# Kernel optimization log

Measured on AMD Instinct MI355X. Metric: run time of the kernel, lower is better.

## Reference

```python
import jax, jax.numpy as jnp
import numpy as np
from jax import lax

DIM = 512
HEADS = 8


def _branch(x, w1, wd):
    # 1x1 pointwise conv (no bias)
    y = jnp.einsum('oc,bchw->bohw', w1, x)
    # ReflectionPad2d(2)
    y = jnp.pad(y, ((0, 0), (0, 0), (2, 2), (2, 2)), mode='reflect')
    # depthwise 3x3, dilation 2, valid padding (net: same spatial size)
    y = lax.conv_general_dilated(
        y, wd, window_strides=(1, 1), padding='VALID', rhs_dilation=(2, 2),
        dimension_numbers=('NCHW', 'OIHW', 'NCHW'), feature_group_count=y.shape[1])
    return y


def setup_inputs() -> dict:
    key = jax.random.key(0)
    ks = jax.random.split(key, 8)
    s = 0.02
    style_feat = jax.random.normal(ks[0], (16, DIM, 64, 64), dtype=jnp.float32)
    fw1 = jax.random.normal(ks[1], (DIM, DIM), dtype=jnp.float32) * s
    fwd_ = jax.random.normal(ks[2], (DIM, 1, 3, 3), dtype=jnp.float32) * s
    gw1 = jax.random.normal(ks[3], (DIM, DIM), dtype=jnp.float32) * s
    gwd = jax.random.normal(ks[4], (DIM, 1, 3, 3), dtype=jnp.float32) * s
    hw1 = jax.random.normal(ks[5], (DIM, DIM), dtype=jnp.float32) * s
    hwd = jax.random.normal(ks[6], (DIM, 1, 3, 3), dtype=jnp.float32) * s
    ow = jax.random.normal(ks[7], (DIM, DIM), dtype=jnp.float32) * s
    temperature = jnp.ones((HEADS, 1, 1), dtype=jnp.float32)
    return dict(style_feat=style_feat, fw1=fw1, fwd_=fwd_, gw1=gw1, gwd=gwd,
                hw1=hw1, hwd=hwd, ow=ow, temperature=temperature)


def reference(style_feat, fw1, fwd_, gw1, gwd, hw1, hwd, ow, temperature):
    B, C, H, W = style_feat.shape
    cph = C // HEADS
    f_x = _branch(style_feat, fw1, fwd_)
    g_x = _branch(style_feat, gw1, gwd)
    h_x = _branch(style_feat, hw1, hwd)
    q = f_x.reshape(B, HEADS, cph, H * W)
    k = g_x.reshape(B, HEADS, cph, H * W)
    v = h_x.reshape(B, HEADS, cph, H * W)
    # channel-wise attention: [B,h,cph,cph]
    energy = jnp.einsum('bhcn,bhdn->bhcd', q, k)
    attn = jax.nn.softmax(energy * temperature[None], axis=-1)
    out = jnp.einsum('bhcd,bhdn->bhcn', attn, v).reshape(B, C, H, W)
    out = jnp.einsum('oc,bchw->bohw', ow, out)
    return out + style_feat
```

## Files before the change

kernel.cpp:

```cpp
#include <hip/hip_runtime.h>

typedef unsigned short u16;
typedef __bf16 bf8_t __attribute__((ext_vector_type(8)));
typedef short short8 __attribute__((ext_vector_type(8)));
typedef float f32x4 __attribute__((ext_vector_type(4)));

#define DEV __device__ __forceinline__

DEV u16 f2bf(float x) {
  unsigned u = __builtin_bit_cast(unsigned, x);
  return (u16)((u + 0x7FFFu + ((u >> 16) & 1u)) >> 16);
}
DEV float bf2f(u16 x) {
  unsigned u = (unsigned)x << 16;
  return __builtin_bit_cast(float, u);
}

DEV void gload16(const u16* g, u16* l) {
  __builtin_amdgcn_global_load_lds((__attribute__((address_space(1))) void*)(g),
                                   (__attribute__((address_space(3))) void*)(l), 16, 0, 0);
}

__global__ void k_wconv(const float* __restrict__ f, const float* __restrict__ g,
                        const float* __restrict__ h, u16* __restrict__ out) {
  int i = blockIdx.x * 256 + threadIdx.x;
  float v;
  if (i < 262144) v = f[i];
  else if (i < 524288) v = g[i - 262144];
  else v = h[i - 524288];
  out[i] = f2bf(v);
}

__global__ __launch_bounds__(256) void k_xt(const float* __restrict__ style, u16* __restrict__ Xt) {
  __shared__ float t[32][33];
  int b = blockIdx.z, c0 = blockIdx.y * 32, n0 = blockIdx.x * 32;
  int tid = threadIdx.x, lr = tid >> 5, lc = tid & 31;
  const float* src = style + ((size_t)b * 512 + c0) * 4096 + n0;
#pragma unroll
  for (int it = 0; it < 4; ++it) {
    int r = it * 8 + lr;
    t[r][lc] = src[(size_t)r * 4096 + lc];
  }
  __syncthreads();
  u16* dst = Xt + ((size_t)b * 4096 + n0) * 512 + c0;
#pragma unroll
  for (int it = 0; it < 4; ++it) {
    int n = it * 8 + lr;
    dst[(size_t)n * 512 + lc] = f2bf(t[lc][n]);
  }
}

DEV void stage_tile(const u16* __restrict__ src, int row0, int kb,
                    u16* lds, int wave, int lane) {
#pragma unroll
  for (int qq = 0; qq < 2; ++qq) {
    int idx = (wave * 2 + qq) * 64 + lane;
    int r = idx >> 2;
    int cb = (idx & 3) * 8;
    gload16(src + (size_t)(row0 + r) * 512 + (kb + cb),
            lds + (wave * 2 + qq) * 512);
  }
}

__global__ __launch_bounds__(256, 2) void k_gemm_branch(
    const u16* __restrict__ Wall, const u16* __restrict__ Xt, u16* __restrict__ Y) {
  int bid = blockIdx.x;
  int xcd = bid & 7, idx = bid >> 3;
  int bh = idx / 384;
  int r = idx - bh * 384;
  int b = xcd * 2 + bh;
  int nt = r / 12, mt = r - nt * 12;
  int M0 = mt * 128, N0 = nt * 128;
  const u16* A = Wall;
  const u16* B = Xt + (size_t)b * (4096 * 512);
  u16* C = Y + (size_t)b * (1536 * 4096);
  int tid = threadIdx.x, wave = tid >> 6, lane = tid & 63;
  int wm = wave >> 1, wn = wave & 1;
  __shared__ __align__(16) u16 lA[2][128 * 32];
  __shared__ __align__(16) u16 lB[2][128 * 32];
  f32x4 acc[4][4];
#pragma unroll
  for (int m = 0; m < 4; ++m)
#pragma unroll
    for (int n = 0; n < 4; ++n) acc[m][n] = (f32x4){0.f, 0.f, 0.f, 0.f};
  stage_tile(A, M0, 0, &lA[0][0], wave, lane);
  stage_tile(B, N0, 0, &lB[0][0], wave, lane);
  __syncthreads();
  int lrow = lane & 15, lk = (lane >> 4) * 8;
#pragma unroll 2
  for (int kt = 0; kt < 16; ++kt) {
    int cur = kt & 1;
    if (kt < 15) {
      stage_tile(A, M0, (kt + 1) * 32, &lA[cur ^ 1][0], wave, lane);
      stage_tile(B, N0, (kt + 1) * 32, &lB[cur ^ 1][0], wave, lane);
    }
    bf8_t af[4], bff[4];
#pragma unroll
    for (int m = 0; m < 4; ++m)
      af[m] = *(const bf8_t*)&lA[cur][(wm * 64 + m * 16 + lrow) * 32 + lk];
#pragma unroll
    for (int n = 0; n < 4; ++n)
      bff[n] = *(const bf8_t*)&lB[cur][(wn * 64 + n * 16 + lrow) * 32 + lk];
#pragma unroll
    for (int m = 0; m < 4; ++m)
#pragma unroll
      for (int n = 0; n < 4; ++n)
        acc[m][n] = __builtin_amdgcn_mfma_f32_16x16x32_bf16(af[m], bff[n], acc[m][n], 0, 0, 0);
    __syncthreads();
  }
  int orow = (lane >> 4) * 4, ocol = lane & 15;
#pragma unroll
  for (int m = 0; m < 4; ++m)
#pragma unroll
    for (int n = 0; n < 4; ++n) {
      int row = M0 + wm * 64 + m * 16 + orow;
      int col = N0 + wn * 64 + n * 16 + ocol;
      u16* cp = C + (size_t)row * 4096 + col;
#pragma unroll
      for (int i = 0; i < 4; ++i) cp[(size_t)i * 4096] = f2bf(acc[m][n][i]);
    }
}

template <typename F>
DEV void dw_row(const u16* plane, const float* w9, int y, F&& store) {
  short8 raw[3][8];
#pragma unroll
  for (int i = 0; i < 3; ++i) {
    int yy = y + 2 * i - 2;
    yy = yy < 0 ? -yy : (yy > 63 ? 126 - yy : yy);
    const short8* rp = (const short8*)(plane + yy * 64);
#pragma unroll
    for (int ch = 0; ch < 8; ++ch) raw[i][ch] = rp[ch];
  }
#pragma unroll
  for (int g = 0; g < 4; ++g) {
    float fr[3][20];
#pragma unroll
    for (int t = 0; t < 20; ++t) {
      int p = g * 16 - 2 + t;
      int rp2 = p < 0 ? -p : (p > 63 ? 126 - p : p);
#pragma unroll
      for (int i = 0; i < 3; ++i)
        fr[i][t] = bf2f((u16)raw[i][rp2 >> 3][rp2 & 7]);
    }
    float o[16];
#pragma unroll
    for (int e = 0; e < 16; ++e) {
      float s = 0.f;
#pragma unroll
      for (int i = 0; i < 3; ++i)
#pragma unroll
        for (int j = 0; j < 3; ++j)
          s += w9[i * 3 + j] * fr[i][e + 2 * j];
      o[e] = s;
    }
    store(g, o);
  }
}

__global__ __launch_bounds__(256, 2) void k_dwE(const u16* __restrict__ Y,
    const float* __restrict__ fwd, const float* __restrict__ gwd, float* __restrict__ E) {
  int band = blockIdx.x, h = blockIdx.y, b = blockIdx.z;
  __shared__ __align__(16) u16 qbuf[64 * 256];
  __shared__ __align__(16) u16 kbuf[64 * 256];
  int tid = threadIdx.x;
  int c = ((tid >> 5) << 3) | (tid & 7);
  int yl = (tid >> 3) & 3;
  int wv = tid >> 6, lane = tid & 63;
  int lrow = lane & 15, lkg = lane >> 4;
  const u16* qp = Y + ((size_t)b * 1536 + h * 64 + c) * 4096;
  const u16* kp = Y + ((size_t)b * 1536 + 512 + h * 64 + c) * 4096;
  float wq9[9], wk9[9];
#pragma unroll
  for (int t = 0; t < 9; ++t) {
    wq9[t] = fwd[(h * 64 + c) * 9 + t];
    wk9[t] = gwd[(h * 64 + c) * 9 + t];
  }
  f32x4 acc[4];
#pragma unroll
  for (int n = 0; n < 4; ++n) acc[n] = (f32x4){0.f, 0.f, 0.f, 0.f};
  char* qrow = (char*)qbuf + c * 512;
  char* krow = (char*)kbuf + c * 512;
  int c7 = c & 7;
#pragma unroll 1
  for (int sb = 0; sb < 4; ++sb) {
    int y = band * 16 + sb * 4 + yl;
    dw_row(qp, wq9, y, [&](int g, const float* o) {
      short8 s0, s1;
#pragma unroll
      for (int e = 0; e < 8; ++e) { s0[e] = (short)f2bf(o[e]); s1[e] = (short)f2bf(o[e + 8]); }
      int ch0 = yl * 8 + g * 2;
      *(short8*)(qrow + 16 * (ch0 ^ c7)) = s0;
      *(short8*)(qrow + 16 * ((ch0 + 1) ^ c7)) = s1;
    });
    dw_row(kp, wk9, y, [&](int g, const float* o) {
      short8 s0, s1;
#pragma unroll
      for (int e = 0; e < 8; ++e) { s0[e] = (short)f2bf(o[e]); s1[e] = (short)f2bf(o[e + 8]); }
      int ch0 = yl * 8 + g * 2;
      *(short8*)(krow + 16 * (ch0 ^ c7)) = s0;
      *(short8*)(krow + 16 * ((ch0 + 1) ^ c7)) = s1;
    });
    __syncthreads();
    const char* qb = (const char*)qbuf + (wv * 16 + lrow) * 512;
    int ca7 = (wv * 16 + lrow) & 7;
#pragma unroll
    for (int ks = 0; ks < 8; ++ks) {
      bf8_t aF = *(const bf8_t*)(qb + 16 * ((ks * 4 + lkg) ^ ca7));
#pragma unroll
      for (int n = 0; n < 4; ++n) {
        int cb = n * 16 + lrow;
        bf8_t bF = *(const bf8_t*)((const char*)kbuf + cb * 512 + 16 * ((ks * 4 + lkg) ^ (cb & 7)));
        acc[n] = __builtin_amdgcn_mfma_f32_16x16x32_bf16(aF, bF, acc[n], 0, 0, 0);
      }
    }
    __syncthreads();
  }
  float* Eo = E + (((size_t)band * 16 + b) * 8 + h) * 4096;
  int orow = (lane >> 4) * 4, ocol = lane & 15;
#pragma unroll
  for (int n = 0; n < 4; ++n)
#pragma unroll
    for (int i = 0; i < 4; ++i)
      Eo[(wv * 16 + orow + i) * 64 + n * 16 + ocol] = acc[n][i];
}

__global__ __launch_bounds__(256, 2) void k_dwV(const u16* __restrict__ Y,
    const float* __restrict__ hwd, u16* __restrict__ Vt) {
  int band = blockIdx.x, ct = blockIdx.y, b = blockIdx.z;
  __shared__ float vb[256 * 68];
  int tid = threadIdx.x;
  int c = ((tid >> 5) << 3) | (tid & 7);
  int yl = (tid >> 3) & 3;
  int cg = tid & 7;
  int cglob = ct * 64 + c;
  const u16* plane = Y + ((size_t)b * 1536 + 1024 + cglob) * 4096;
  float w9[9];
#pragma unroll
  for (int t = 0; t < 9; ++t) w9[t] = hwd[cglob * 9 + t];
#pragma unroll 1
  for (int sb = 0; sb < 4; ++sb) {
    int y = band * 16 + sb * 4 + yl;
    dw_row(plane, w9, y, [&](int g, const float* o) {
#pragma unroll
      for (int e = 0; e < 16; ++e)
        vb[((g * 16 + e) * 4 + yl) * 68 + c] = o[e];
    });
    __syncthreads();
#pragma unroll
    for (int k = 0; k < 8; ++k) {
      int np = (tid >> 3) + 32 * k;
      int x = np >> 2, yy = np & 3;
      int ng = (band * 16 + sb * 4 + yy) * 64 + x;
      f32x4 r0 = *(const f32x4*)&vb[np * 68 + cg * 8];
      f32x4 r1 = *(const f32x4*)&vb[np * 68 + cg * 8 + 4];
      short8 s;
#pragma unroll
      for (int e = 0; e < 4; ++e) { s[e] = (short)f2bf(r0[e]); s[e + 4] = (short)f2bf(r1[e]); }
      *(short8*)(Vt + ((size_t)b * 4096 + ng) * 512 + ct * 64 + cg * 8) = s;
    }
    __syncthreads();
  }
}

__global__ __launch_bounds__(64) void k_softmax(float* __restrict__ E, const float* __restrict__ temp) {
  int bh = blockIdx.x;
  int b = bh >> 3, h = bh & 7;
  int c = threadIdx.x;
  float* p0 = E + (((size_t)b * 8 + h) * 64 + c) * 64;
  float tv = temp[h];
  float e[64];
  float mx = -1e30f;
#pragma unroll
  for (int d = 0; d < 64; ++d) {
    float v = (p0[d] + p0[d + 524288] + p0[d + 1048576] + p0[d + 1572864]) * tv;
    e[d] = v;
    mx = fmaxf(mx, v);
  }
  float s = 0.f;
#pragma unroll
  for (int d = 0; d < 64; ++d) { float v = __expf(e[d] - mx); e[d] = v; s += v; }
  float inv = 1.f / s;
#pragma unroll
  for (int d = 0; d < 64; ++d) p0[d] = e[d] * inv;
}

__global__ __launch_bounds__(256) void k_m2(const float* __restrict__ E, const float* __restrict__ ow,
                                            u16* __restrict__ M2) {
  int og = blockIdx.x, h = blockIdx.y, b = blockIdx.z;
  __shared__ float at[4096];
  int tid = threadIdx.x;
  const float* attn = E + ((size_t)b * 8 + h) * 4096;
  for (int v = tid; v < 4096; v += 256) at[v] = attn[v];
  __syncthreads();
  int o = og * 64 + (tid >> 2), dq = (tid & 3) * 16;
  const float* owr = ow + (size_t)o * 512 + h * 64;
  float acc[16];
#pragma unroll
  for (int e = 0; e < 16; ++e) acc[e] = 0.f;
  for (int cc = 0; cc < 64; ++cc) {
    float wv = owr[cc];
#pragma unroll
    for (int e = 0; e < 16; ++e) acc[e] += wv * at[cc * 64 + dq + e];
  }
  u16* dst = M2 + ((size_t)b * 512 + o) * 512 + h * 64 + dq;
  short8 s0, s1;
#pragma unroll
  for (int e = 0; e < 8; ++e) { s0[e] = (short)f2bf(acc[e]); s1[e] = (short)f2bf(acc[e + 8]); }
  *(short8*)dst = s0;
  *(short8*)(dst + 8) = s1;
}

__global__ __launch_bounds__(256, 2) void k_gemm_final(
    const u16* __restrict__ M2, const u16* __restrict__ Vt,
    const float* __restrict__ style, float* __restrict__ out) {
  int b = blockIdx.z;
  const u16* A = M2 + (size_t)b * (512 * 512);
  const u16* B = Vt + (size_t)b * (4096 * 512);
  const float* st = style + (size_t)b * (512 * 4096);
  float* op = out + (size_t)b * (512 * 4096);
  int M0 = blockIdx.y * 128, N0 = blockIdx.x * 128;
  int tid = threadIdx.x, wave = tid >> 6, lane = tid & 63;
  int wm = wave >> 1, wn = wave & 1;
  __shared__ __align__(16) u16 lA[2][128 * 32];
  __shared__ __align__(16) u16 lB[2][128 * 32];
  f32x4 acc[4][4];
#pragma unroll
  for (int m = 0; m < 4; ++m)
#pragma unroll
    for (int n = 0; n < 4; ++n) acc[m][n] = (f32x4){0.f, 0.f, 0.f, 0.f};
  stage_tile(A, M0, 0, &lA[0][0], wave, lane);
  stage_tile(B, N0, 0, &lB[0][0], wave, lane);
  __syncthreads();
  int lrow = lane & 15, lk = (lane >> 4) * 8;
#pragma unroll 2
  for (int kt = 0; kt < 16; ++kt) {
    int cur = kt & 1;
    if (kt < 15) {
      stage_tile(A, M0, (kt + 1) * 32, &lA[cur ^ 1][0], wave, lane);
      stage_tile(B, N0, (kt + 1) * 32, &lB[cur ^ 1][0], wave, lane);
    }
    bf8_t af[4], bff[4];
#pragma unroll
    for (int m = 0; m < 4; ++m)
      af[m] = *(const bf8_t*)&lA[cur][(wm * 64 + m * 16 + lrow) * 32 + lk];
#pragma unroll
    for (int n = 0; n < 4; ++n)
      bff[n] = *(const bf8_t*)&lB[cur][(wn * 64 + n * 16 + lrow) * 32 + lk];
#pragma unroll
    for (int m = 0; m < 4; ++m)
#pragma unroll
      for (int n = 0; n < 4; ++n)
        acc[m][n] = __builtin_amdgcn_mfma_f32_16x16x32_bf16(af[m], bff[n], acc[m][n], 0, 0, 0);
    __syncthreads();
  }
  int orow = (lane >> 4) * 4, ocol = lane & 15;
#pragma unroll
  for (int m = 0; m < 4; ++m)
#pragma unroll
    for (int n = 0; n < 4; ++n) {
      int row = M0 + wm * 64 + m * 16 + orow;
      int col = N0 + wn * 64 + n * 16 + ocol;
      float* cp = op + (size_t)row * 4096 + col;
      const float* sp = st + (size_t)row * 4096 + col;
#pragma unroll
      for (int i = 0; i < 4; ++i) cp[(size_t)i * 4096] = acc[m][n][i] + sp[(size_t)i * 4096];
    }
}


extern "C" void kernel_launch(void* const* d_in, const int* in_sizes, int n_in,
                              void* d_out, int out_size, void* d_ws, size_t ws_size,
                              hipStream_t stream) {
  const float* style = (const float*)d_in[0];
  const float* fw1   = (const float*)d_in[1];
  const float* fwd_  = (const float*)d_in[2];
  const float* gw1   = (const float*)d_in[3];
  const float* gwd   = (const float*)d_in[4];
  const float* hw1   = (const float*)d_in[5];
  const float* hwd   = (const float*)d_in[6];
  const float* ow    = (const float*)d_in[7];
  const float* temp  = (const float*)d_in[8];
  float* out = (float*)d_out;

  char* ws = (char*)d_ws;
  u16*   Wbf = (u16*)(ws + 0);
  u16*   Y   = (u16*)(ws + (size_t)2097152);
  u16*   Xt  = (u16*)(ws + (size_t)203423744);
  u16*   Vt  = Xt;
  float* E   = (float*)(ws + (size_t)270532608);
  u16*   M2  = (u16*)(ws + (size_t)278921216);

  k_wconv<<<3072, 256, 0, stream>>>(fw1, gw1, hw1, Wbf);
  k_xt<<<dim3(128, 16, 16), 256, 0, stream>>>(style, Xt);
  k_gemm_branch<<<6144, 256, 0, stream>>>(Wbf, Xt, Y);
  k_dwE<<<dim3(4, 8, 16), 256, 0, stream>>>(Y, fwd_, gwd, E);
  k_dwV<<<dim3(4, 8, 16), 256, 0, stream>>>(Y, hwd, Vt);
  k_softmax<<<128, 64, 0, stream>>>(E, temp);
  k_m2<<<dim3(8, 8, 16), 256, 0, stream>>>(E, ow, M2);
  k_gemm_final<<<dim3(32, 4, 16), 256, 0, stream>>>(M2, Vt, style, out);
}
```

Baseline: 408.4 us.

## Vectorize conversions, fuse softmax into M2 kernel, simplify branch GEMM grid

Vectorizes the weight fp32-to-bf16 conversion and the transposed bf16 store in k_xt to use 4-wide accesses. Fuses the softmax and attention-times-output-weight kernels into one, keeping the normalized attention in shared memory and saving a launch and a global round trip. Replaces the XCD-aware block swizzle in the branch GEMM with a plain 3D grid, which may change L2 locality. The fused kernel launches only 128 blocks, so the M2 stage has far less parallelism.

```diff
diff --git a/kernel.cpp b/kernel.cpp
--- a/kernel.cpp
+++ b/kernel.cpp
@@ -3,6 +3,7 @@
 typedef unsigned short u16;
 typedef __bf16 bf8_t __attribute__((ext_vector_type(8)));
 typedef short short8 __attribute__((ext_vector_type(8)));
+typedef u16 u16x4 __attribute__((ext_vector_type(4)));
 typedef float f32x4 __attribute__((ext_vector_type(4)));
 
 #define DEV __device__ __forceinline__
@@ -23,12 +24,13 @@
 
 __global__ void k_wconv(const float* __restrict__ f, const float* __restrict__ g,
                         const float* __restrict__ h, u16* __restrict__ out) {
-  int i = blockIdx.x * 256 + threadIdx.x;
-  float v;
-  if (i < 262144) v = f[i];
-  else if (i < 524288) v = g[i - 262144];
-  else v = h[i - 524288];
-  out[i] = f2bf(v);
+  int i4 = (blockIdx.x * 256 + threadIdx.x) * 4;
+  const float* src = (i4 < 262144) ? (f + i4) : (i4 < 524288) ? (g + i4 - 262144) : (h + i4 - 524288);
+  f32x4 v = *(const f32x4*)src;
+  u16x4 o;
+#pragma unroll
+  for (int e = 0; e < 4; ++e) o[e] = f2bf(v[e]);
+  *(u16x4*)(out + i4) = o;
 }
 
 __global__ __launch_bounds__(256) void k_xt(const float* __restrict__ style, u16* __restrict__ Xt) {
@@ -42,12 +44,11 @@
     t[r][lc] = src[(size_t)r * 4096 + lc];
   }
   __syncthreads();
-  u16* dst = Xt + ((size_t)b * 4096 + n0) * 512 + c0;
-#pragma unroll
-  for (int it = 0; it < 4; ++it) {
-    int n = it * 8 + lr;
-    dst[(size_t)n * 512 + lc] = f2bf(t[lc][n]);
-  }
+  int cs = (tid & 7) * 4, n = tid >> 3;
+  u16x4 s;
+#pragma unroll
+  for (int j = 0; j < 4; ++j) s[j] = f2bf(t[cs + j][n]);
+  *(u16x4*)(Xt + ((size_t)b * 4096 + n0 + n) * 512 + c0 + cs) = s;
 }
 
 DEV void stage_tile(const u16* __restrict__ src, int row0, int kb,
@@ -64,13 +65,9 @@
 
 __global__ __launch_bounds__(256, 2) void k_gemm_branch(
     const u16* __restrict__ Wall, const u16* __restrict__ Xt, u16* __restrict__ Y) {
-  int bid = blockIdx.x;
-  int xcd = bid & 7, idx = bid >> 3;
-  int bh = idx / 384;
-  int r = idx - bh * 384;
-  int b = xcd * 2 + bh;
-  int nt = r / 12, mt = r - nt * 12;
-  int M0 = mt * 128, N0 = nt * 128;
+  int z = blockIdx.z;
+  int t = z >> 4, b = z & 15;
+  int M0 = t * 512 + blockIdx.y * 128, N0 = blockIdx.x * 128;
   const u16* A = Wall;
   const u16* B = Xt + (size_t)b * (4096 * 512);
   u16* C = Y + (size_t)b * (1536 * 4096);
@@ -263,52 +260,51 @@
   }
 }
 
-__global__ __launch_bounds__(64) void k_softmax(float* __restrict__ E, const float* __restrict__ temp) {
-  int bh = blockIdx.x;
-  int b = bh >> 3, h = bh & 7;
-  int c = threadIdx.x;
-  float* p0 = E + (((size_t)b * 8 + h) * 64 + c) * 64;
-  float tv = temp[h];
-  float e[64];
-  float mx = -1e30f;
-#pragma unroll
-  for (int d = 0; d < 64; ++d) {
-    float v = (p0[d] + p0[d + 524288] + p0[d + 1048576] + p0[d + 1572864]) * tv;
-    e[d] = v;
-    mx = fmaxf(mx, v);
-  }
-  float s = 0.f;
-#pragma unroll
-  for (int d = 0; d < 64; ++d) { float v = __expf(e[d] - mx); e[d] = v; s += v; }
-  float inv = 1.f / s;
-#pragma unroll
-  for (int d = 0; d < 64; ++d) p0[d] = e[d] * inv;
-}
-
-__global__ __launch_bounds__(256) void k_m2(const float* __restrict__ E, const float* __restrict__ ow,
-                                            u16* __restrict__ M2) {
-  int og = blockIdx.x, h = blockIdx.y, b = blockIdx.z;
+__global__ __launch_bounds__(256) void k_sm2(const float* __restrict__ E,
+    const float* __restrict__ temp, const float* __restrict__ ow, u16* __restrict__ M2) {
+  int h = blockIdx.x, b = blockIdx.y;
   __shared__ float at[4096];
   int tid = threadIdx.x;
-  const float* attn = E + ((size_t)b * 8 + h) * 4096;
-  for (int v = tid; v < 4096; v += 256) at[v] = attn[v];
+  if (tid < 64) {
+    int c = tid;
+    const float* pr = E + (((size_t)b * 8 + h) * 64 + c) * 64;
+    float tv = temp[h];
+    float e[64];
+    float mx = -1e30f;
+#pragma unroll
+    for (int d = 0; d < 64; ++d) {
+      float v = (pr[d] + pr[d + 524288] + pr[d + 1048576] + pr[d + 1572864]) * tv;
+      e[d] = v;
+      mx = fmaxf(mx, v);
+    }
+    float s = 0.f;
+#pragma unroll
+    for (int d = 0; d < 64; ++d) { float v = __expf(e[d] - mx); e[d] = v; s += v; }
+    float inv = 1.f / s;
+#pragma unroll
+    for (int d = 0; d < 64; ++d) at[c * 64 + d] = e[d] * inv;
+  }
   __syncthreads();
-  int o = og * 64 + (tid >> 2), dq = (tid & 3) * 16;
-  const float* owr = ow + (size_t)o * 512 + h * 64;
-  float acc[16];
-#pragma unroll
-  for (int e = 0; e < 16; ++e) acc[e] = 0.f;
-  for (int cc = 0; cc < 64; ++cc) {
-    float wv = owr[cc];
-#pragma unroll
-    for (int e = 0; e < 16; ++e) acc[e] += wv * at[cc * 64 + dq + e];
-  }
-  u16* dst = M2 + ((size_t)b * 512 + o) * 512 + h * 64 + dq;
-  short8 s0, s1;
-#pragma unroll
-  for (int e = 0; e < 8; ++e) { s0[e] = (short)f2bf(acc[e]); s1[e] = (short)f2bf(acc[e + 8]); }
-  *(short8*)dst = s0;
-  *(short8*)(dst + 8) = s1;
+  int o4 = tid >> 2, dq = (tid & 3) * 16;
+#pragma unroll 1
+  for (int og = 0; og < 8; ++og) {
+    int o = og * 64 + o4;
+    const float* owr = ow + (size_t)o * 512 + h * 64;
+    float acc[16];
+#pragma unroll
+    for (int e = 0; e < 16; ++e) acc[e] = 0.f;
+    for (int cc = 0; cc < 64; ++cc) {
+      float wv = owr[cc];
+#pragma unroll
+      for (int e = 0; e < 16; ++e) acc[e] += wv * at[cc * 64 + dq + e];
+    }
+    u16* dst = M2 + ((size_t)b * 512 + o) * 512 + h * 64 + dq;
+    short8 s0, s1;
+#pragma unroll
+    for (int e = 0; e < 8; ++e) { s0[e] = (short)f2bf(acc[e]); s1[e] = (short)f2bf(acc[e + 8]); }
+    *(short8*)dst = s0;
+    *(short8*)(dst + 8) = s1;
+  }
 }
 
 __global__ __launch_bounds__(256, 2) void k_gemm_final(
@@ -391,12 +387,11 @@
   float* E   = (float*)(ws + (size_t)270532608);
   u16*   M2  = (u16*)(ws + (size_t)278921216);
 
-  k_wconv<<<3072, 256, 0, stream>>>(fw1, gw1, hw1, Wbf);
+  k_wconv<<<768, 256, 0, stream>>>(fw1, gw1, hw1, Wbf);
   k_xt<<<dim3(128, 16, 16), 256, 0, stream>>>(style, Xt);
-  k_gemm_branch<<<6144, 256, 0, stream>>>(Wbf, Xt, Y);
+  k_gemm_branch<<<dim3(32, 4, 48), 256, 0, stream>>>(Wbf, Xt, Y);
   k_dwE<<<dim3(4, 8, 16), 256, 0, stream>>>(Y, fwd_, gwd, E);
   k_dwV<<<dim3(4, 8, 16), 256, 0, stream>>>(Y, hwd, Vt);
-  k_softmax<<<128, 64, 0, stream>>>(E, temp);
-  k_m2<<<dim3(8, 8, 16), 256, 0, stream>>>(E, ow, M2);
+  k_sm2<<<dim3(8, 16), 256, 0, stream>>>(E, temp, ow, M2);
   k_gemm_final<<<dim3(32, 4, 16), 256, 0, stream>>>(M2, Vt, style, out);
 }
```

New measurement: 416.2 us. Within noise of the previous version (+1.9%).
